# Kernel tuning notes

Hardware: AMD Instinct MI355X
Metric: run time of the kernel (lower is better)

## Reference

```python
import jax, jax.numpy as jnp
import numpy as np

N = 8192
E = 262144
H = 64


def setup_inputs() -> dict:
    key = jax.random.key(0)
    ks = jax.random.split(key, 9)
    edge_index = jax.random.randint(ks[0], (2, E), 0, N, dtype=jnp.int64)
    edge_attr = jax.random.uniform(ks[1], (E,), dtype=jnp.float32)
    node_features = jax.random.normal(ks[2], (N, N), dtype=jnp.float32)
    # GCNConv weights (glorot-ish scale) and biases
    W1 = jax.random.normal(ks[3], (N, H), dtype=jnp.float32) / np.sqrt(N)
    b1 = jnp.zeros((H,), dtype=jnp.float32)
    W2 = jax.random.normal(ks[4], (H, H), dtype=jnp.float32) / np.sqrt(H)
    b2 = jnp.zeros((H,), dtype=jnp.float32)
    fcW = jax.random.normal(ks[5], (H, N), dtype=jnp.float32) / np.sqrt(H)
    fcb = jnp.zeros((N,), dtype=jnp.float32)
    return {"edge_index": edge_index, "edge_attr": edge_attr,
            "node_features": node_features,
            "W1": W1, "b1": b1, "W2": W2, "b2": b2,
            "fcW": fcW, "fcb": fcb}


def _gcn_conv(x, W, b, src, dst, ew, n_nodes):
    # PyG GCNConv with edge weights: x' = D^{-1/2} (A + I) D^{-1/2} (x W) + b
    # src/dst/ew already include self-loops (weight 1.0).
    x = x @ W                                        # [N, out]
    deg = jax.ops.segment_sum(ew, dst, num_segments=n_nodes)  # in-degree w/ loops
    dinv = jax.lax.rsqrt(deg)                        # deg >= 1 due to self loops
    norm = dinv[src] * ew * dinv[dst]                # [E+N]
    out = jax.ops.segment_sum(x[src] * norm[:, None], dst, num_segments=n_nodes)
    return out + b


def reference(edge_index, edge_attr, node_features, W1, b1, W2, b2, fcW, fcb):
    n_nodes = node_features.shape[0]
    loops = jnp.arange(n_nodes, dtype=edge_index.dtype)
    src = jnp.concatenate([edge_index[0], loops])
    dst = jnp.concatenate([edge_index[1], loops])
    ew = jnp.concatenate([edge_attr, jnp.ones((n_nodes,), edge_attr.dtype)])
    x = jax.nn.relu(_gcn_conv(node_features, W1, b1, src, dst, ew, n_nodes))
    x = jax.nn.relu(_gcn_conv(x, W2, b2, src, dst, ew, n_nodes))
    x = x @ fcW + fcb
    return jax.nn.softmax(x, axis=-1)
```

## Files before the change

kernel.cpp:

```cpp
#include <hip/hip_runtime.h>


#define NN 8192
#define NE 262144
#define HD 64
#define KCH 1024
#define NKC 8
#define NGR 8

typedef float f32x4 __attribute__((ext_vector_type(4)));
typedef short v8s   __attribute__((ext_vector_type(8)));
typedef unsigned short ushort_t;

__device__ __forceinline__ unsigned short bf16_rne(float f){
  union { float f; unsigned u; } v; v.f = f;
  unsigned r = v.u + 0x7fffu + ((v.u >> 16) & 1u);
  return (unsigned short)(r >> 16);
}
__device__ __forceinline__ float bf16_f32(unsigned short h){
  union { unsigned u; float f; } v; v.u = ((unsigned)h) << 16;
  return v.f;
}
__device__ __forceinline__ f32x4 mfma16(v8s a, v8s b, f32x4 c){
  return __builtin_amdgcn_mfma_f32_16x16x32_bf16(a, b, c, 0, 0, 0);
}
__device__ __forceinline__ void split_tr(float f, short& hi, short& lo){
  unsigned u = __float_as_uint(f);
  hi = (short)(u >> 16);
  float fh = __uint_as_float(u & 0xffff0000u);
  float d = f - fh;
  lo = (short)(__float_as_uint(d) >> 16);
}
__device__ __forceinline__ void gload16(const void* g, void* l){
  __builtin_amdgcn_global_load_lds(
      (const __attribute__((address_space(1))) unsigned int*)g,
      (__attribute__((address_space(3))) unsigned int*)l, 16, 0, 0);
}

__global__ void k_prep0(const float* __restrict__ W1, const float* __restrict__ fcW,
                        ushort_t* w1hi, ushort_t* w1lo, ushort_t* fcwp,
                        float* deg, int* cnt, int* wcnt, float* S){
  int idx = blockIdx.x*blockDim.x + threadIdx.x;
  if (idx < NN){ deg[idx]=1.0f; cnt[idx]=0; wcnt[idx]=0; S[idx]=0.0f; }
  {
    int kk = idx & 31, c = (idx>>5)&15, nt = (idx>>9)&3, kb = idx>>11;
    int k = kb*32 + kk, col = nt*16 + c;
    float w = W1[(size_t)k*HD + col];
    unsigned short hi = bf16_rne(w);
    w1hi[idx] = hi;
    w1lo[idx] = bf16_rne(w - bf16_f32(hi));
  }
  {
    int kk = idx & 31, c = (idx>>5)&15, cblk = (idx>>9)&511, kb = idx>>18;
    int k = kb*32 + kk, col = cblk*16 + c;
    fcwp[idx] = bf16_rne(fcW[(size_t)k*NN + col]);
  }
}

__global__ void k_deg_cnt(const int* ei, const float* ew, float* deg, int* cnt){
  int e = blockIdx.x*blockDim.x + threadIdx.x;
  if (e < NE){
    int d = ei[NE + e];
    atomicAdd(&deg[d], ew[e]);
    atomicAdd(&cnt[d], 1);
  }
}

__global__ void k_scan(const int* cnt, const float* deg, int* rowptr, float* dinv){
  __shared__ int part[256];
  int t = threadIdx.x;
  int loc[32]; int s = 0;
  #pragma unroll
  for (int j=0;j<32;++j){ loc[j] = cnt[t*32+j]; s += loc[j]; }
  part[t] = s; __syncthreads();
  for (int off=1; off<256; off<<=1){
    int v = (t >= off) ? part[t-off] : 0;
    __syncthreads();
    part[t] += v;
    __syncthreads();
  }
  int run = part[t] - s;
  #pragma unroll
  for (int j=0;j<32;++j){ rowptr[t*32+j] = run; run += loc[j]; }
  if (t == 255) rowptr[NN] = run;
  #pragma unroll
  for (int j=0;j<32;++j) dinv[t*32+j] = 1.0f / sqrtf(deg[t*32+j]);
}

__global__ void k_fill(const int* ei, const float* ew, const float* dinv,
                       const int* rowptr, int* wcnt, int* csr_src, float* csr_nrm){
  int e = blockIdx.x*blockDim.x + threadIdx.x;
  if (e < NE){
    int s = ei[e], d = ei[NE+e];
    int slot = rowptr[d] + atomicAdd(&wcnt[d], 1);
    csr_src[slot] = s;
    csr_nrm[slot] = dinv[s] * ew[e] * dinv[d];
  }
}

__global__ __launch_bounds__(256, 1) void k_gemm1(const float* __restrict__ X,
                                                  const ushort_t* __restrict__ w1hi,
                                                  const ushort_t* __restrict__ w1lo,
                                                  float* __restrict__ xw1p){
  extern __shared__ __align__(16) char smem[];
  char* bufA  = smem;
  char* bufBh = smem + 65536;
  char* bufBl = smem + 98304;
  int lane = threadIdx.x & 63, w = threadIdx.x >> 6;
  int r = lane & 15, seg = lane >> 4;
  int l31 = lane & 31, lhi = lane >> 5;
  int row0 = blockIdx.x*64, kb0 = blockIdx.y*KCH;

  const char* Xb = (const char*)X;
  size_t asrc[8];
  #pragma unroll
  for (int i=0;i<8;++i){
    int row = w*16 + 2*i + lhi;
    asrc[i] = (size_t)(row0 + row)*32768 + (size_t)kb0*4
            + (size_t)((l31 ^ (row & 7)) * 16);
  }
  size_t bsrc0 = ((size_t)(kb0 >> 5))*4096 + (size_t)w*4096 + (size_t)lane*16;

  f32x4 z = {0.f,0.f,0.f,0.f};
  f32x4 acc[4] = {z,z,z,z};

  {
    char* aB = bufA + (w*16)*512;
    #pragma unroll
    for (int i=0;i<8;++i) gload16(Xb + asrc[i], aB + i*1024);
    const char* bh = (const char*)w1hi + bsrc0;
    const char* bl = (const char*)w1lo + bsrc0;
    #pragma unroll
    for (int j=0;j<4;++j){
      gload16(bh + j*1024, bufBh + w*4096 + j*1024);
      gload16(bl + j*1024, bufBl + w*4096 + j*1024);
    }
  }
  __syncthreads();

  for (int g = 0; g < NGR; ++g){
    int cur = g & 1;
    if (g + 1 < NGR){
      char* aB = bufA + (cur^1)*32768 + (w*16)*512;
      #pragma unroll
      for (int i=0;i<8;++i) gload16(Xb + asrc[i] + (size_t)(g+1)*512, aB + i*1024);
      const char* bh = (const char*)w1hi + bsrc0 + (size_t)(g+1)*16384;
      const char* bl = (const char*)w1lo + bsrc0 + (size_t)(g+1)*16384;
      char* bhB = bufBh + (cur^1)*16384 + w*4096;
      char* blB = bufBl + (cur^1)*16384 + w*4096;
      #pragma unroll
      for (int j=0;j<4;++j){
        gload16(bh + j*1024, bhB + j*1024);
        gload16(bl + j*1024, blB + j*1024);
      }
    }
    const char* aB  = bufA  + cur*32768 + (w*16 + r)*512;
    const char* bhB = bufBh + cur*16384;
    const char* blB = bufBl + cur*16384;
    #pragma unroll
    for (int tt=0; tt<4; ++tt){
      f32x4 a0 = *(const f32x4*)(aB + (((tt*8 + seg*2    ) ^ (r & 7)) << 4));
      f32x4 a1 = *(const f32x4*)(aB + (((tt*8 + seg*2 + 1) ^ (r & 7)) << 4));
      v8s ah, al;
      #pragma unroll
      for (int j=0;j<4;++j){
        short h,l;
        split_tr(a0[j], h, l); ah[j]   = h; al[j]   = l;
        split_tr(a1[j], h, l); ah[4+j] = h; al[4+j] = l;
      }
      #pragma unroll
      for (int nt=0; nt<4; ++nt){
        int fo = tt*4096 + nt*1024 + r*64 + seg*16;
        v8s bh = *(const v8s*)(bhB + fo);
        v8s bl = *(const v8s*)(blB + fo);
        acc[nt] = mfma16(ah, bh, acc[nt]);
        acc[nt] = mfma16(ah, bl, acc[nt]);
        acc[nt] = mfma16(al, bh, acc[nt]);
      }
    }
    __syncthreads();
  }

  float* o = xw1p + (size_t)blockIdx.y*(NN*HD) + (size_t)(row0 + w*16)*HD;
  #pragma unroll
  for (int nt=0; nt<4; ++nt)
    #pragma unroll
    for (int j=0;j<4;++j)
      o[(4*seg + j)*HD + nt*16 + r] = acc[nt][j];
}

__global__ __launch_bounds__(256) void k_red(const float* __restrict__ xw1p,
                                             float* __restrict__ xw1){
  int i = blockIdx.x*blockDim.x + threadIdx.x;
  f32x4 s = {0.f,0.f,0.f,0.f};
  #pragma unroll
  for (int c=0;c<NKC;++c){
    f32x4 v = *(const f32x4*)(xw1p + (size_t)c*NN*HD + (size_t)i*4);
    s[0]+=v[0]; s[1]+=v[1]; s[2]+=v[2]; s[3]+=v[3];
  }
  *(f32x4*)(xw1 + (size_t)i*4) = s;
}

__global__ __launch_bounds__(256) void k_agg1c(const float* __restrict__ xin,
                                               const float* __restrict__ b1,
                                               const float* __restrict__ W2,
                                               const float* __restrict__ dinv,
                                               const int* __restrict__ rowptr,
                                               const int* __restrict__ csr_src,
                                               const float* __restrict__ csr_nrm,
                                               float* __restrict__ x2w){
  __shared__ float W2s[64*64];
  __shared__ float rows[4][64];
  int lane = threadIdx.x & 63, w = threadIdx.x >> 6;
  for (int o = threadIdx.x; o < 64*64; o += 256) W2s[o] = W2[o];
  __syncthreads();

  int i = blockIdx.x*4 + w;
  float di = dinv[i];
  float acc = di*di * xin[(size_t)i*HD + lane];
  int e = rowptr[i], e1 = rowptr[i+1];
  for (; e + 1 < e1; e += 2){
    int s0 = csr_src[e], s1 = csr_src[e+1];
    float n0 = csr_nrm[e], n1 = csr_nrm[e+1];
    acc += n0 * xin[(size_t)s0*HD + lane];
    acc += n1 * xin[(size_t)s1*HD + lane];
  }
  if (e < e1) acc += csr_nrm[e] * xin[(size_t)csr_src[e]*HD + lane];
  float v = acc + b1[lane];
  rows[w][lane] = v > 0.f ? v : 0.f;
  __syncthreads();

  float acc2 = 0.f;
  #pragma unroll
  for (int k=0;k<64;++k) acc2 += rows[w][k] * W2s[k*64 + lane];
  x2w[(size_t)i*HD + lane] = acc2;
}

__global__ __launch_bounds__(256) void k_agg2(const float* __restrict__ xin,
                                              const float* __restrict__ b2,
                                              const float* __restrict__ dinv,
                                              const int* __restrict__ rowptr,
                                              const int* __restrict__ csr_src,
                                              const float* __restrict__ csr_nrm,
                                              ushort_t* __restrict__ x2b){
  int lane = threadIdx.x & 63, w = threadIdx.x >> 6;
  int i = blockIdx.x*4 + w;
  float di = dinv[i];
  float acc = di*di * xin[(size_t)i*HD + lane];
  int e = rowptr[i], e1 = rowptr[i+1];
  for (; e + 1 < e1; e += 2){
    int s0 = csr_src[e], s1 = csr_src[e+1];
    float n0 = csr_nrm[e], n1 = csr_nrm[e+1];
    acc += n0 * xin[(size_t)s0*HD + lane];
    acc += n1 * xin[(size_t)s1*HD + lane];
  }
  if (e < e1) acc += csr_nrm[e] * xin[(size_t)csr_src[e]*HD + lane];
  float v = acc + b2[lane];
  v = v > 0.f ? v : 0.f;
  x2b[(size_t)i*HD + lane] = bf16_rne(v);
}

__global__ __launch_bounds__(256) void k_rowsum(const ushort_t* __restrict__ x2b,
                                                const ushort_t* __restrict__ fcwp,
                                                const float* __restrict__ fcb,
                                                float* __restrict__ S){
  int lane = threadIdx.x & 63, w = threadIdx.x >> 6;
  int r = lane & 15, seg = lane >> 4;
  int row0 = blockIdx.x*128 + w*32;
  const ushort_t* xb = x2b + (size_t)(row0 + r)*HD + seg*8;
  v8s x00 = *(const v8s*)(xb);
  v8s x01 = *(const v8s*)(xb + 32);
  v8s x10 = *(const v8s*)(xb + 16*HD);
  v8s x11 = *(const v8s*)(xb + 16*HD + 32);
  float rp0 = 0.f, rp1 = 0.f;
  for (int cb=0; cb<4; ++cb){
    int colbase = blockIdx.y*256 + cb*64;
    f32x4 z = {0.f,0.f,0.f,0.f};
    f32x4 acc0[4] = {z,z,z,z}, acc1[4] = {z,z,z,z};
    #pragma unroll
    for (int nt=0; nt<4; ++nt){
      int cblk = (colbase >> 4) + nt;
      v8s bA = *(const v8s*)(fcwp + ((size_t)cblk*16 + r)*32 + seg*8);
      v8s bB = *(const v8s*)(fcwp + ((size_t)(512 + cblk)*16 + r)*32 + seg*8);
      acc0[nt] = mfma16(bA, x00, acc0[nt]);
      acc0[nt] = mfma16(bB, x01, acc0[nt]);
      acc1[nt] = mfma16(bA, x10, acc1[nt]);
      acc1[nt] = mfma16(bB, x11, acc1[nt]);
    }
    #pragma unroll
    for (int nt=0; nt<4; ++nt){
      int col = colbase + nt*16 + seg*4;
      f32x4 fb = *(const f32x4*)(fcb + col);
      #pragma unroll
      for (int j=0;j<4;++j){
        rp0 += __expf(acc0[nt][j] + fb[j]);
        rp1 += __expf(acc1[nt][j] + fb[j]);
      }
    }
  }
  rp0 += __shfl_xor(rp0, 16); rp0 += __shfl_xor(rp0, 32);
  rp1 += __shfl_xor(rp1, 16); rp1 += __shfl_xor(rp1, 32);
  if (lane < 16){
    atomicAdd(&S[row0 + lane],      rp0);
    atomicAdd(&S[row0 + 16 + lane], rp1);
  }
}

__global__ __launch_bounds__(256) void k_passB(const ushort_t* __restrict__ x2b,
                                               const ushort_t* __restrict__ fcwp,
                                               const float* __restrict__ fcb,
                                               const float* __restrict__ S,
                                               float* __restrict__ out){
  int lane = threadIdx.x & 63, w = threadIdx.x >> 6;
  int r = lane & 15, seg = lane >> 4;
  int row0 = blockIdx.x*128 + w*32;
  const ushort_t* xb = x2b + (size_t)(row0 + r)*HD + seg*8;
  v8s x00 = *(const v8s*)(xb);
  v8s x01 = *(const v8s*)(xb + 32);
  v8s x10 = *(const v8s*)(xb + 16*HD);
  v8s x11 = *(const v8s*)(xb + 16*HD + 32);
  float si0 = 1.0f / S[row0 + r];
  float si1 = 1.0f / S[row0 + 16 + r];
  float* o0 = out + (size_t)(row0 + r)*NN;
  float* o1 = out + (size_t)(row0 + 16 + r)*NN;
  for (int cb=0; cb<4; ++cb){
    int colbase = blockIdx.y*256 + cb*64;
    f32x4 z = {0.f,0.f,0.f,0.f};
    f32x4 acc0[4] = {z,z,z,z}, acc1[4] = {z,z,z,z};
    #pragma unroll
    for (int nt=0; nt<4; ++nt){
      int cblk = (colbase >> 4) + nt;
      v8s bA = *(const v8s*)(fcwp + ((size_t)cblk*16 + r)*32 + seg*8);
      v8s bB = *(const v8s*)(fcwp + ((size_t)(512 + cblk)*16 + r)*32 + seg*8);
      acc0[nt] = mfma16(bA, x00, acc0[nt]);
      acc0[nt] = mfma16(bB, x01, acc0[nt]);
      acc1[nt] = mfma16(bA, x10, acc1[nt]);
      acc1[nt] = mfma16(bB, x11, acc1[nt]);
    }
    #pragma unroll
    for (int nt=0; nt<4; ++nt){
      int col = colbase + nt*16 + seg*4;
      f32x4 fb = *(const f32x4*)(fcb + col);
      f32x4 v0, v1;
      #pragma unroll
      for (int j=0;j<4;++j){
        v0[j] = __expf(acc0[nt][j] + fb[j]) * si0;
        v1[j] = __expf(acc1[nt][j] + fb[j]) * si1;
      }
      *(f32x4*)(o0 + col) = v0;
      *(f32x4*)(o1 + col) = v1;
    }
  }
}

extern "C" void kernel_launch(void* const* d_in, const int* in_sizes, int n_in,
                              void* d_out, int out_size, void* d_ws, size_t ws_size,
                              hipStream_t stream){
  (void)in_sizes; (void)n_in; (void)out_size; (void)ws_size;
  const int*   ei  = (const int*)  d_in[0];
  const float* ew  = (const float*)d_in[1];
  const float* X   = (const float*)d_in[2];
  const float* W1  = (const float*)d_in[3];
  const float* b1  = (const float*)d_in[4];
  const float* W2  = (const float*)d_in[5];
  const float* b2  = (const float*)d_in[6];
  const float* fcW = (const float*)d_in[7];
  const float* fcb = (const float*)d_in[8];
  float* out = (float*)d_out;
  char*  ws  = (char*)d_ws;

  float*    deg     = (float*)   (ws + 0);
  float*    dinv    = (float*)   (ws + 32768);
  int*      cnt     = (int*)     (ws + 65536);
  int*      wcnt    = (int*)     (ws + 98304);
  int*      rowptr  = (int*)     (ws + 131072);
  int*      csr_src = (int*)     (ws + 167936);
  float*    csr_nrm = (float*)   (ws + 1216512);
  ushort_t* w1hi    = (ushort_t*)(ws + 2265088);
  ushort_t* w1lo    = (ushort_t*)(ws + 3313664);
  ushort_t* fcwp    = (ushort_t*)(ws + 4362240);
  float*    xw1p    = (float*)   (ws + 5410816);
  float*    xw1     = (float*)   (ws + 22188032);
  float*    x2w     = (float*)   (ws + 24285184);
  ushort_t* x2b     = (ushort_t*)(ws + 26382336);
  float*    S       = (float*)   (ws + 27430912);

  static bool attr_set = false;
  if (!attr_set){
    hipFuncSetAttribute((const void*)k_gemm1,
                        hipFuncAttributeMaxDynamicSharedMemorySize, 131072);
    attr_set = true;
  }

  k_prep0   <<<2048, 256, 0, stream>>>(W1, fcW, w1hi, w1lo, fcwp, deg, cnt, wcnt, S);
  k_deg_cnt <<<1024, 256, 0, stream>>>(ei, ew, deg, cnt);
  k_scan    <<<1,    256, 0, stream>>>(cnt, deg, rowptr, dinv);
  k_fill    <<<1024, 256, 0, stream>>>(ei, ew, dinv, rowptr, wcnt, csr_src, csr_nrm);
  k_gemm1   <<<dim3(128, NKC), 256, 131072, stream>>>(X, w1hi, w1lo, xw1p);
  k_red     <<<512,  256, 0, stream>>>(xw1p, xw1);
  k_agg1c   <<<2048, 256, 0, stream>>>(xw1, b1, W2, dinv, rowptr, csr_src, csr_nrm, x2w);
  k_agg2    <<<2048, 256, 0, stream>>>(x2w, b2, dinv, rowptr, csr_src, csr_nrm, x2b);
  k_rowsum  <<<dim3(64,32), 256, 0, stream>>>(x2b, fcwp, fcb, S);
  k_passB   <<<dim3(64,32), 256, 0, stream>>>(x2b, fcwp, fcb, S, out);
}
```

Baseline: 305.2 us.

## Swizzle W1 LDS layout and use partial vmcnt waits in split-bf16 GEMM1

The prep kernel now stores the hi/lo bf16 W1 tiles with an XOR-swizzled 16-byte chunk order, so B-fragment reads from LDS avoid bank conflicts. The GEMM1 main loop is restructured around a STAGE lambda with precomputed A/B LDS offsets. The full __syncthreads is replaced by an explicit s_waitcnt vmcnt(16) plus raw s_barrier, so the next stage's global-to-LDS loads stay in flight while the current tile is computed. The hand-written waitcnt depends on the exact count of outstanding loads and is fragile if the compiler reorders or adds memory ops.

```diff
diff --git a/kernel.cpp b/kernel.cpp
--- a/kernel.cpp
+++ b/kernel.cpp
@@ -6,7 +6,8 @@
 #define HD 64
 #define KCH 1024
 #define NKC 8
-#define NGR 8
+#define KSTEP 128
+#define NT (KCH/KSTEP)
 
 typedef float f32x4 __attribute__((ext_vector_type(4)));
 typedef short v8s   __attribute__((ext_vector_type(8)));
@@ -47,8 +48,10 @@
     int k = kb*32 + kk, col = nt*16 + c;
     float w = W1[(size_t)k*HD + col];
     unsigned short hi = bf16_rne(w);
-    w1hi[idx] = hi;
-    w1lo[idx] = bf16_rne(w - bf16_f32(hi));
+    int chunk = idx >> 3, e = idx & 7;
+    int sidx = ((chunk ^ (c & 7)) << 3) | e;
+    w1hi[sidx] = hi;
+    w1lo[sidx] = bf16_rne(w - bf16_f32(hi));
   }
   {
     int kk = idx & 31, c = (idx>>5)&15, cblk = (idx>>9)&511, kb = idx>>18;
@@ -103,9 +106,6 @@
                                                   const ushort_t* __restrict__ w1lo,
                                                   float* __restrict__ xw1p){
   extern __shared__ __align__(16) char smem[];
-  char* bufA  = smem;
-  char* bufBh = smem + 65536;
-  char* bufBl = smem + 98304;
   int lane = threadIdx.x & 63, w = threadIdx.x >> 6;
   int r = lane & 15, seg = lane >> 4;
   int l31 = lane & 31, lhi = lane >> 5;
@@ -115,52 +115,62 @@
   size_t asrc[8];
   #pragma unroll
   for (int i=0;i<8;++i){
-    int row = w*16 + 2*i + lhi;
-    asrc[i] = (size_t)(row0 + row)*32768 + (size_t)kb0*4
-            + (size_t)((l31 ^ (row & 7)) * 16);
-  }
-  size_t bsrc0 = ((size_t)(kb0 >> 5))*4096 + (size_t)w*4096 + (size_t)lane*16;
+    int rl = w*16 + 2*i + lhi;
+    int cs = (l31 & 24) | ((l31 ^ rl) & 7);
+    asrc[i] = (size_t)(row0 + rl)*(NN*4) + (size_t)kb0*4 + (size_t)cs*16;
+  }
+  const char* bhBase = (const char*)w1hi;
+  const char* blBase = (const char*)w1lo;
+
+  int aoff[4][2];
+  #pragma unroll
+  for (int ks=0; ks<4; ++ks)
+    #pragma unroll
+    for (int j=0; j<2; ++j)
+      aoff[ks][j] = (w*16 + r)*512 + (ks*8 + (((seg*2 + j) ^ r) & 7))*16;
+  int bc[4];
+  #pragma unroll
+  for (int nt=0; nt<4; ++nt)
+    bc[nt] = ((nt*64 + r*4 + seg) ^ (r & 7)) << 4;
 
   f32x4 z = {0.f,0.f,0.f,0.f};
   f32x4 acc[4] = {z,z,z,z};
 
-  {
-    char* aB = bufA + (w*16)*512;
-    #pragma unroll
-    for (int i=0;i<8;++i) gload16(Xb + asrc[i], aB + i*1024);
-    const char* bh = (const char*)w1hi + bsrc0;
-    const char* bl = (const char*)w1lo + bsrc0;
-    #pragma unroll
-    for (int j=0;j<4;++j){
-      gload16(bh + j*1024, bufBh + w*4096 + j*1024);
-      gload16(bl + j*1024, bufBl + w*4096 + j*1024);
-    }
-  }
-  __syncthreads();
-
-  for (int g = 0; g < NGR; ++g){
-    int cur = g & 1;
-    if (g + 1 < NGR){
-      char* aB = bufA + (cur^1)*32768 + (w*16)*512;
-      #pragma unroll
-      for (int i=0;i<8;++i) gload16(Xb + asrc[i] + (size_t)(g+1)*512, aB + i*1024);
-      const char* bh = (const char*)w1hi + bsrc0 + (size_t)(g+1)*16384;
-      const char* bl = (const char*)w1lo + bsrc0 + (size_t)(g+1)*16384;
-      char* bhB = bufBh + (cur^1)*16384 + w*4096;
-      char* blB = bufBl + (cur^1)*16384 + w*4096;
-      #pragma unroll
-      for (int j=0;j<4;++j){
-        gload16(bh + j*1024, bhB + j*1024);
-        gload16(bl + j*1024, blB + j*1024);
-      }
-    }
-    const char* aB  = bufA  + cur*32768 + (w*16 + r)*512;
-    const char* bhB = bufBh + cur*16384;
-    const char* blB = bufBl + cur*16384;
-    #pragma unroll
-    for (int tt=0; tt<4; ++tt){
-      f32x4 a0 = *(const f32x4*)(aB + (((tt*8 + seg*2    ) ^ (r & 7)) << 4));
-      f32x4 a1 = *(const f32x4*)(aB + (((tt*8 + seg*2 + 1) ^ (r & 7)) << 4));
+  auto STAGE = [&](int t, int b){
+    char* aD = smem + b*32768 + (w*8)*1024;
+    size_t ko = (size_t)t*512;
+    #pragma unroll
+    for (int i=0;i<8;++i)
+      gload16(Xb + asrc[i] + ko, aD + i*1024);
+    size_t sB = (size_t)((kb0 >> 5) + t*4 + w) * 4096;
+    char* hD = smem + 65536 + b*16384 + w*4096;
+    char* lD = smem + 98304 + b*16384 + w*4096;
+    #pragma unroll
+    for (int i=0;i<4;++i){
+      gload16(bhBase + sB + i*1024 + lane*16, hD + i*1024);
+      gload16(blBase + sB + i*1024 + lane*16, lD + i*1024);
+    }
+  };
+
+  STAGE(0, 0);
+
+  for (int t = 0; t < NT; ++t){
+    int cur = t & 1;
+    if (t + 1 < NT){
+      STAGE(t+1, cur^1);
+      asm volatile("s_waitcnt vmcnt(16)" ::: "memory");
+    } else {
+      asm volatile("s_waitcnt vmcnt(0)" ::: "memory");
+    }
+    __builtin_amdgcn_s_barrier();
+    __builtin_amdgcn_sched_barrier(0);
+    const char* A  = smem + cur*32768;
+    const char* Bh = smem + 65536 + cur*16384;
+    const char* Bl = smem + 98304 + cur*16384;
+    #pragma unroll
+    for (int ks=0; ks<4; ++ks){
+      f32x4 a0 = *(const f32x4*)(A + aoff[ks][0]);
+      f32x4 a1 = *(const f32x4*)(A + aoff[ks][1]);
       v8s ah, al;
       #pragma unroll
       for (int j=0;j<4;++j){
@@ -170,15 +180,15 @@
       }
       #pragma unroll
       for (int nt=0; nt<4; ++nt){
-        int fo = tt*4096 + nt*1024 + r*64 + seg*16;
-        v8s bh = *(const v8s*)(bhB + fo);
-        v8s bl = *(const v8s*)(blB + fo);
+        v8s bh = *(const v8s*)(Bh + ks*4096 + bc[nt]);
+        v8s bl = *(const v8s*)(Bl + ks*4096 + bc[nt]);
         acc[nt] = mfma16(ah, bh, acc[nt]);
         acc[nt] = mfma16(ah, bl, acc[nt]);
         acc[nt] = mfma16(al, bh, acc[nt]);
       }
     }
-    __syncthreads();
+    __builtin_amdgcn_sched_barrier(0);
+    __builtin_amdgcn_s_barrier();
   }
 
   float* o = xw1p + (size_t)blockIdx.y*(NN*HD) + (size_t)(row0 + w*16)*HD;
```

New measurement: 285.2 us. 6.5% less time.
